# Kernel optimization log

Measured on AMD Instinct MI355X. Metric: run time of the kernel, lower is better.

The kernel has to match this reference:

```python
import jax, jax.numpy as jnp
import numpy as np

B, C, H, W = 4, 256, 64, 64
C8 = C // 8


def _xavier(key, shape):
    fan_in, fan_out = shape[1], shape[0]
    limit = float(np.sqrt(6.0 / (fan_in + fan_out)))
    return jax.random.uniform(key, shape, jnp.float32, -limit, limit)


def setup_inputs() -> dict:
    key = jax.random.key(0)
    ks = jax.random.split(key, 10)
    inp = {
        "x": jax.random.normal(ks[0], (B, C, H, W), jnp.float32),
        "y": jax.random.normal(ks[1], (B, C, H, W), jnp.float32),
        "Wfx": _xavier(ks[2], (C8, C)), "bfx": jnp.zeros((C8,), jnp.float32),
        "Wgx": _xavier(ks[3], (C8, C)), "bgx": jnp.zeros((C8,), jnp.float32),
        "Whx": _xavier(ks[4], (C, C)),  "bhx": jnp.zeros((C,), jnp.float32),
        "Wfy": _xavier(ks[5], (C8, C)), "bfy": jnp.zeros((C8,), jnp.float32),
        "Wgy": _xavier(ks[6], (C8, C)), "bgy": jnp.zeros((C8,), jnp.float32),
        "Why": _xavier(ks[7], (C, C)),  "bhy": jnp.zeros((C,), jnp.float32),
        # torch init is gamma=0 which zeroes the attention branch; use a random
        # scalar so the reference exercises the full computation.
        "gamma": jax.random.normal(ks[8], (1,), jnp.float32),
    }
    return inp


def _conv1x1(x, Wt, b):
    # 1x1 conv == per-pixel linear over channels; output flattened to [B, O, N]
    b_, c, h, w = x.shape
    out = jnp.einsum('oc,bchw->bohw', Wt, x) + b[None, :, None, None]
    return out.reshape(b_, -1, h * w)


def reference(x, y, Wfx, bfx, Wgx, bgx, Whx, bhx, Wfy, bfy, Wgy, bgy, Why, bhy, gamma):
    b, c, h, w = x.shape
    fx = _conv1x1(x, Wfx, bfx)  # [B, C8, N]
    gx = _conv1x1(x, Wgx, bgx)
    hx = _conv1x1(x, Whx, bhx)  # [B, C, N]
    fy = _conv1x1(y, Wfy, bfy)
    gy = _conv1x1(y, Wgy, bgy)
    hy = _conv1x1(y, Why, bhy)

    # attention_x = softmax(f_y^T @ g_x) over last dim; [B, N, N]
    att_x = jax.nn.softmax(jnp.einsum('bcn,bcm->bnm', fy, gx), axis=-1)
    att_y = jax.nn.softmax(jnp.einsum('bcn,bcm->bnm', fx, gy), axis=-1)

    sa_x = jnp.einsum('bcn,bnm->bcm', hx, att_x).reshape(b, c, h, w)
    sa_y = jnp.einsum('bcn,bnm->bcm', hy, att_y).reshape(b, c, h, w)

    out_x = gamma[0] * sa_x + x
    out_y = gamma[0] * sa_y + y
    return (out_x, out_y)
```

## Files before the change

kernel.cpp:

```cpp
#include <hip/hip_runtime.h>

#define BB 4
#define CC 256
#define NN 4096

typedef _Float16 half_t;
typedef __attribute__((ext_vector_type(8))) _Float16 half8;
typedef __attribute__((ext_vector_type(4))) _Float16 half4;
typedef __attribute__((ext_vector_type(4))) float floatx4;
typedef __attribute__((ext_vector_type(16))) float floatx16;

__global__ __launch_bounds__(256)
void cvt_w_kernel(const float* __restrict__ Wfx, const float* __restrict__ Wgx,
                  const float* __restrict__ Whx, const float* __restrict__ Wfy,
                  const float* __restrict__ Wgy, const float* __restrict__ Why,
                  half_t* __restrict__ oWfx, half_t* __restrict__ oWgx,
                  half_t* __restrict__ oWhx, half_t* __restrict__ oWfy,
                  half_t* __restrict__ oWgy, half_t* __restrict__ oWhy)
{
    const float* src; half_t* dst; int n;
    switch (blockIdx.y) {
        case 0: src = Wfx; dst = oWfx; n = 32 * CC; break;
        case 1: src = Wgx; dst = oWgx; n = 32 * CC; break;
        case 2: src = Whx; dst = oWhx; n = CC * CC; break;
        case 3: src = Wfy; dst = oWfy; n = 32 * CC; break;
        case 4: src = Wgy; dst = oWgy; n = 32 * CC; break;
        default: src = Why; dst = oWhy; n = CC * CC; break;
    }
    int idx = (blockIdx.x * 256 + threadIdx.x) * 4;
    if (idx >= n) return;
    float4 v = *(const float4*)&src[idx];
    half4 h; h[0] = (half_t)v.x; h[1] = (half_t)v.y; h[2] = (half_t)v.z; h[3] = (half_t)v.w;
    *(half4*)&dst[idx] = h;
}

__global__ __launch_bounds__(512, 4)
void prep_kernel(const float* __restrict__ x, const float* __restrict__ y,
                 const half_t* __restrict__ Wfx, const half_t* __restrict__ Wgx,
                 const half_t* __restrict__ Whx, const half_t* __restrict__ Wfy,
                 const half_t* __restrict__ Wgy, const half_t* __restrict__ Why,
                 const float* __restrict__ bfx, const float* __restrict__ bgx,
                 const float* __restrict__ bhx, const float* __restrict__ bfy,
                 const float* __restrict__ bgy, const float* __restrict__ bhy,
                 half_t* __restrict__ fxT, half_t* __restrict__ gxT,
                 half_t* __restrict__ hx,
                 half_t* __restrict__ fyT, half_t* __restrict__ gyT,
                 half_t* __restrict__ hy)
{
    __shared__ half_t xT[64][266];

    const int n0 = blockIdx.x * 64;
    const int b  = blockIdx.y;
    const int sel = blockIdx.z;
    const float* in = sel ? y : x;
    const half_t* Wf = sel ? Wfy : Wfx;
    const half_t* Wg = sel ? Wgy : Wgx;
    const half_t* Wh = sel ? Why : Whx;
    const float*  bf = sel ? bfy : bfx;
    const float*  bg = sel ? bgy : bgx;
    const float*  bh = sel ? bhy : bhx;
    half_t* fT = sel ? fyT : fxT;
    half_t* gT = sel ? gyT : gxT;
    half_t* h  = sel ? hy : hx;

    const int t = threadIdx.x;
    const int w = t >> 6, lane = t & 63;
    const int q = lane >> 4, mc = lane & 15;

    {
        const int n4 = t & 15;
        const int cb = t >> 4;
        const float* inb = in + (size_t)b * CC * NN + n0 + n4 * 4;
        #pragma unroll
        for (int j = 0; j < 8; ++j) {
            const int c = cb + 32 * j;
            float4 v = *(const float4*)&inb[(size_t)c * NN];
            xT[n4 * 4 + 0][c] = (half_t)v.x;
            xT[n4 * 4 + 1][c] = (half_t)v.y;
            xT[n4 * 4 + 2][c] = (half_t)v.z;
            xT[n4 * 4 + 3][c] = (half_t)v.w;
        }
    }
    __syncthreads();

    {
        const int of  = w >> 1;
        const int col = (of & 1) * 16 + mc;
        const half_t* Ws = (of < 2) ? Wf : Wg;
        const float*  bs = (of < 2) ? bf : bg;
        half_t* dst = (of < 2) ? fT : gT;
        const float bv = bs[col];
        floatx4 accf[2] = {{bv, bv, bv, bv}, {bv, bv, bv, bv}};

        #pragma unroll
        for (int ks = 0; ks < 8; ++ks) {
            int k0 = ks * 32 + q * 8;
            half8 bfr = *(const half8*)&Ws[(size_t)col * CC + k0];
            #pragma unroll
            for (int e = 0; e < 2; ++e) {
                half8 af = *(const half8*)&xT[(w & 1) * 32 + e * 16 + mc][k0];
                accf[e] = __builtin_amdgcn_mfma_f32_16x16x32_f16(af, bfr, accf[e], 0, 0, 0);
            }
        }
        #pragma unroll
        for (int e = 0; e < 2; ++e)
            #pragma unroll
            for (int r = 0; r < 4; ++r) {
                int n = n0 + (w & 1) * 32 + e * 16 + q * 4 + r;
                dst[((size_t)b * NN + n) * 32 + col] = (half_t)accf[e][r];
            }
    }

    {
        const int o0 = w * 32;
        floatx4 acch[2][4];
        #pragma unroll
        for (int j = 0; j < 2; ++j) {
            floatx4 bv;
            #pragma unroll
            for (int r = 0; r < 4; ++r) bv[r] = bh[o0 + j * 16 + q * 4 + r];
            #pragma unroll
            for (int i = 0; i < 4; ++i) acch[j][i] = bv;
        }

        #pragma unroll
        for (int ks = 0; ks < 8; ++ks) {
            int k0 = ks * 32 + q * 8;
            half8 a0 = *(const half8*)&Wh[(size_t)(o0 + mc) * CC + k0];
            half8 a1 = *(const half8*)&Wh[(size_t)(o0 + 16 + mc) * CC + k0];
            #pragma unroll
            for (int i = 0; i < 4; ++i) {
                half8 bfr = *(const half8*)&xT[i * 16 + mc][k0];
                acch[0][i] = __builtin_amdgcn_mfma_f32_16x16x32_f16(a0, bfr, acch[0][i], 0, 0, 0);
                acch[1][i] = __builtin_amdgcn_mfma_f32_16x16x32_f16(a1, bfr, acch[1][i], 0, 0, 0);
            }
        }

        half_t* hb = h + (size_t)b * CC * NN;
        #pragma unroll
        for (int j = 0; j < 2; ++j)
            #pragma unroll
            for (int i = 0; i < 4; ++i)
                #pragma unroll
                for (int r = 0; r < 4; ++r) {
                    int o = o0 + j * 16 + q * 4 + r;
                    hb[(size_t)o * NN + n0 + i * 16 + mc] = (half_t)acch[j][i][r];
                }
    }
}

__global__ __launch_bounds__(256)
void stats_kernel(const half_t* __restrict__ fT0, const half_t* __restrict__ gT0,
                  const half_t* __restrict__ fT1, const half_t* __restrict__ gT1,
                  float* __restrict__ L0, float* __restrict__ L1)
{
    __shared__ float red_l[4][32];
    const int b  = blockIdx.y;
    const int sel = blockIdx.z;
    const half_t* fT = sel ? fT1 : fT0;
    const half_t* gT = sel ? gT1 : gT0;
    float* Lout = sel ? L1 : L0;

    const int n0 = blockIdx.x * 32;
    const int t  = threadIdx.x;
    const int w = t >> 6, lane = t & 63, q = lane >> 4, mc = lane & 15;
    const half_t* fTb = fT + (size_t)b * NN * 32;
    const half_t* gTb = gT + (size_t)b * NN * 32;

    half8 a0 = *(const half8*)&fTb[(size_t)(n0 + mc) * 32 + q * 8];
    half8 a1 = *(const half8*)&fTb[(size_t)(n0 + 16 + mc) * 32 + q * 8];

    float l0[4] = {0.f, 0.f, 0.f, 0.f}, l1[4] = {0.f, 0.f, 0.f, 0.f};
    for (int it = 0; it < NN / 64; ++it) {
        int m = (it * 4 + w) * 16 + mc;
        half8 bfr = *(const half8*)&gTb[(size_t)m * 32 + q * 8];
        floatx4 S0 = __builtin_amdgcn_mfma_f32_16x16x32_f16(a0, bfr, (floatx4){0.f,0.f,0.f,0.f}, 0, 0, 0);
        floatx4 S1 = __builtin_amdgcn_mfma_f32_16x16x32_f16(a1, bfr, (floatx4){0.f,0.f,0.f,0.f}, 0, 0, 0);
        #pragma unroll
        for (int r = 0; r < 4; ++r) { l0[r] += __expf(S0[r]); l1[r] += __expf(S1[r]); }
    }
    #pragma unroll
    for (int r = 0; r < 4; ++r) {
        #pragma unroll
        for (int off = 1; off < 16; off <<= 1) {
            l0[r] += __shfl_xor(l0[r], off);
            l1[r] += __shfl_xor(l1[r], off);
        }
    }
    if (mc == 0)
        #pragma unroll
        for (int r = 0; r < 4; ++r) {
            red_l[w][q * 4 + r]      = l0[r];
            red_l[w][16 + q * 4 + r] = l1[r];
        }
    __syncthreads();
    if (t < 32) {
        float L = red_l[0][t] + red_l[1][t] + red_l[2][t] + red_l[3][t];
        Lout[(size_t)b * NN + n0 + t] = -log2f(L);
    }
}

__global__ __launch_bounds__(512, 4)
void pv_kernel(const half_t* __restrict__ fT0, const half_t* __restrict__ gT0,
               const half_t* __restrict__ h0, const float* __restrict__ L0,
               const float* __restrict__ src0, float* __restrict__ out0,
               const half_t* __restrict__ fT1, const half_t* __restrict__ gT1,
               const half_t* __restrict__ h1, const float* __restrict__ L1,
               const float* __restrict__ src1, float* __restrict__ out1,
               const float* __restrict__ gamma)
{
    __shared__ half_t h_lds[256][72];
    __shared__ half_t PT[2][64][72];

    const int m0 = blockIdx.x * 64;
    const int b  = blockIdx.y & 3;
    const int sel = blockIdx.y >> 2;
    const half_t* fT = sel ? fT1 : fT0;
    const half_t* gT = sel ? gT1 : gT0;
    const half_t* h  = sel ? h1 : h0;
    const float*  Lg = sel ? L1 : L0;
    const float*  src = sel ? src1 : src0;
    float* out = sel ? out1 : out0;

    const int t = threadIdx.x;
    const int w = t >> 6, lane = t & 63;
    const int q = lane >> 4, mc = lane & 15;
    const int l5 = lane >> 5, l31 = lane & 31;

    const int mg  = (w >> 1) * 16;
    const int nhf = (w & 1) * 32;

    const half_t* fTb = fT + (size_t)b * NN * 32;
    const half_t* gTb = gT + (size_t)b * NN * 32;
    const half_t* hb  = h + (size_t)b * CC * NN;
    const float*  Lb  = Lg + (size_t)b * NN;

    const half8 gS = *(const half8*)&gTb[(size_t)(m0 + mg + mc) * 32 + q * 8];

    const int srow = t >> 3;
    const int sch  = t & 7;

    const half_t* hP = hb + (size_t)srow * NN + sch * 8;
    const half_t* fP = fTb + (size_t)(nhf + mc) * 32 + q * 8;
    const float*  lP = Lb + nhf + q * 4;

    floatx16 acc[2];
    #pragma unroll
    for (int bm = 0; bm < 2; ++bm)
        #pragma unroll
        for (int r = 0; r < 16; ++r) acc[bm][r] = 0.f;

    half8 hpre[4];
    half8 fu[2], ff[2];
    floatx4 lvu[2], lvf[2];

    {
        half8 f0[2]; floatx4 l0[2];
        #pragma unroll
        for (int s = 0; s < 2; ++s) {
            f0[s] = *(const half8*)&fP[(size_t)(s * 16) * 32];
            l0[s] = *(const floatx4*)&lP[s * 16];
        }
        #pragma unroll
        for (int s = 0; s < 2; ++s) {
            floatx4 S = __builtin_amdgcn_mfma_f32_16x16x32_f16(
                f0[s], gS, (floatx4){0.f, 0.f, 0.f, 0.f}, 0, 0, 0);
            half4 p;
            p[0] = (half_t)exp2f(fmaf(S[0], 1.44269504f, l0[s][0]));
            p[1] = (half_t)exp2f(fmaf(S[1], 1.44269504f, l0[s][1]));
            p[2] = (half_t)exp2f(fmaf(S[2], 1.44269504f, l0[s][2]));
            p[3] = (half_t)exp2f(fmaf(S[3], 1.44269504f, l0[s][3]));
            *(half4*)&PT[0][mg + mc][nhf + s * 16 + q * 4] = p;
        }
    }
    #pragma unroll
    for (int i = 0; i < 4; ++i)
        hpre[i] = *(const half8*)&hP[(size_t)(64 * i) * NN];
    #pragma unroll
    for (int s = 0; s < 2; ++s) {
        fu[s]  = *(const half8*)&fP[(size_t)(64 + s * 16) * 32];
        lvu[s] = *(const floatx4*)&lP[64 + s * 16];
    }

    #pragma unroll 2
    for (int T = 0; T < NN / 64; ++T) {
        const int cur = T & 1, nxt = cur ^ 1;

        __syncthreads();
        #pragma unroll
        for (int i = 0; i < 4; ++i)
            *(half8*)&h_lds[srow + 64 * i][sch * 8] = hpre[i];
        __syncthreads();

        int ntn  = (T + 1) * 64; if (ntn  >= NN) ntn  = 0;
        int ntn2 = (T + 2) * 64; if (ntn2 >= NN) ntn2 -= NN;
        #pragma unroll
        for (int i = 0; i < 4; ++i)
            hpre[i] = *(const half8*)&hP[(size_t)(64 * i) * NN + ntn];
        #pragma unroll
        for (int s = 0; s < 2; ++s) {
            ff[s]  = *(const half8*)&fP[(size_t)(ntn2 + s * 16) * 32];
            lvf[s] = *(const floatx4*)&lP[ntn2 + s * 16];
        }

        #pragma unroll
        for (int s = 0; s < 2; ++s) {
            floatx4 S = __builtin_amdgcn_mfma_f32_16x16x32_f16(
                fu[s], gS, (floatx4){0.f, 0.f, 0.f, 0.f}, 0, 0, 0);
            half4 p;
            p[0] = (half_t)exp2f(fmaf(S[0], 1.44269504f, lvu[s][0]));
            p[1] = (half_t)exp2f(fmaf(S[1], 1.44269504f, lvu[s][1]));
            p[2] = (half_t)exp2f(fmaf(S[2], 1.44269504f, lvu[s][2]));
            p[3] = (half_t)exp2f(fmaf(S[3], 1.44269504f, lvu[s][3]));
            *(half4*)&PT[nxt][mg + mc][nhf + s * 16 + q * 4] = p;
        }

        __builtin_amdgcn_s_setprio(1);
        #pragma unroll
        for (int ch = 0; ch < 4; ++ch) {
            half8 Ah = *(const half8*)&h_lds[w * 32 + l31][ch * 16 + l5 * 8];
            half8 B0 = *(const half8*)&PT[cur][l31][ch * 16 + l5 * 8];
            half8 B1 = *(const half8*)&PT[cur][32 + l31][ch * 16 + l5 * 8];
            acc[0] = __builtin_amdgcn_mfma_f32_32x32x16_f16(Ah, B0, acc[0], 0, 0, 0);
            acc[1] = __builtin_amdgcn_mfma_f32_32x32x16_f16(Ah, B1, acc[1], 0, 0, 0);
        }
        __builtin_amdgcn_s_setprio(0);

        #pragma unroll
        for (int s = 0; s < 2; ++s) { fu[s] = ff[s]; lvu[s] = lvf[s]; }
    }

    const float gm = gamma[0];
    const float* srcb = src + (size_t)b * CC * NN;
    float* outb = out + (size_t)b * CC * NN;
    #pragma unroll
    for (int bm = 0; bm < 2; ++bm) {
        const int m = m0 + bm * 32 + l31;
        #pragma unroll
        for (int r = 0; r < 16; ++r) {
            int c = w * 32 + (r & 3) + 8 * (r >> 2) + 4 * l5;
            size_t idx = (size_t)c * NN + m;
            outb[idx] = fmaf(gm, acc[bm][r], srcb[idx]);
        }
    }
}

extern "C" void kernel_launch(void* const* d_in, const int* in_sizes, int n_in,
                              void* d_out, int out_size, void* d_ws, size_t ws_size,
                              hipStream_t stream)
{
    const float* x   = (const float*)d_in[0];
    const float* y   = (const float*)d_in[1];
    const float* Wfx = (const float*)d_in[2];
    const float* bfx = (const float*)d_in[3];
    const float* Wgx = (const float*)d_in[4];
    const float* bgx = (const float*)d_in[5];
    const float* Whx = (const float*)d_in[6];
    const float* bhx = (const float*)d_in[7];
    const float* Wfy = (const float*)d_in[8];
    const float* bfy = (const float*)d_in[9];
    const float* Wgy = (const float*)d_in[10];
    const float* bgy = (const float*)d_in[11];
    const float* Why = (const float*)d_in[12];
    const float* bhy = (const float*)d_in[13];
    const float* gam = (const float*)d_in[14];

    const size_t SZ_XT = (size_t)BB * NN * CC;
    const size_t SZ_FG = (size_t)BB * NN * 32;
    half_t* xTx   = (half_t*)d_ws;
    half_t* xTy   = xTx + SZ_XT;
    half_t* hx    = xTy + SZ_XT;
    half_t* hy    = hx + SZ_XT;
    half_t* fxT   = hy + SZ_XT;
    half_t* gxT   = fxT + SZ_FG;
    half_t* fyT   = gxT + SZ_FG;
    half_t* gyT   = fyT + SZ_FG;
    half_t* Wfx_h = gyT + SZ_FG;
    half_t* Wgx_h = Wfx_h + 32 * CC;
    half_t* Wfy_h = Wgx_h + 32 * CC;
    half_t* Wgy_h = Wfy_h + 32 * CC;
    half_t* Whx_h = Wgy_h + 32 * CC;
    half_t* Why_h = Whx_h + CC * CC;
    float*  Lx    = (float*)(Why_h + CC * CC);
    float*  Ly    = Lx + (size_t)BB * NN;

    float* outx = (float*)d_out;
    float* outy = outx + (size_t)BB * CC * NN;

    cvt_w_kernel<<<dim3(64, 6), 256, 0, stream>>>(Wfx, Wgx, Whx, Wfy, Wgy, Why,
                                                  Wfx_h, Wgx_h, Whx_h, Wfy_h, Wgy_h, Why_h);

    prep_kernel<<<dim3(64, 4, 2), 512, 0, stream>>>(
        x, y, Wfx_h, Wgx_h, Whx_h, Wfy_h, Wgy_h, Why_h,
        bfx, bgx, bhx, bfy, bgy, bhy,
        fxT, gxT, hx, fyT, gyT, hy);

    stats_kernel<<<dim3(128, 4, 2), 256, 0, stream>>>(fyT, gxT, fxT, gyT, Lx, Ly);

    pv_kernel<<<dim3(64, 8), 512, 0, stream>>>(
        fyT, gxT, hx, Lx, x, outx,
        fxT, gyT, hy, Ly, y, outy, gam);
}
```

Before: 253.4 us.

## Double the PV kernel output tile to 128 columns to reuse staged h tiles

The PV kernel now covers 128 output positions per block instead of 64. Each wave computes a 2x2 grid of 32x32 MFMA tiles, and the QK/exp stage produces two 16-row slices per wave. This halves how often the h tile is reloaded from global memory per output and raises MFMA work per LDS load. In exchange the grid shrinks to 256 blocks, the launch bound drops to 2 blocks per CU, and more accumulator registers and LDS are used per block, so latency hiding may get worse.

```diff
diff --git a/kernel.cpp b/kernel.cpp
--- a/kernel.cpp
+++ b/kernel.cpp
@@ -200,7 +200,7 @@
     }
 }
 
-__global__ __launch_bounds__(512, 4)
+__global__ __launch_bounds__(512, 2)
 void pv_kernel(const half_t* __restrict__ fT0, const half_t* __restrict__ gT0,
                const half_t* __restrict__ h0, const float* __restrict__ L0,
                const float* __restrict__ src0, float* __restrict__ out0,
@@ -210,9 +210,9 @@
                const float* __restrict__ gamma)
 {
     __shared__ half_t h_lds[256][72];
-    __shared__ half_t PT[2][64][72];
-
-    const int m0 = blockIdx.x * 64;
+    __shared__ half_t PT[2][128][72];
+
+    const int m0 = blockIdx.x * 128;
     const int b  = blockIdx.y & 3;
     const int sel = blockIdx.y >> 2;
     const half_t* fT = sel ? fT1 : fT0;
@@ -227,28 +227,34 @@
     const int q = lane >> 4, mc = lane & 15;
     const int l5 = lane >> 5, l31 = lane & 31;
 
-    const int mg  = (w >> 1) * 16;
-    const int nhf = (w & 1) * 32;
+    const int smg = (w >> 1) * 32;
+    const int snh = (w & 1) * 32;
+    const int cg  = (w & 3) * 64;
+    const int pmg = (w >> 2) * 64;
 
     const half_t* fTb = fT + (size_t)b * NN * 32;
     const half_t* gTb = gT + (size_t)b * NN * 32;
     const half_t* hb  = h + (size_t)b * CC * NN;
     const float*  Lb  = Lg + (size_t)b * NN;
 
-    const half8 gS = *(const half8*)&gTb[(size_t)(m0 + mg + mc) * 32 + q * 8];
+    half8 gS[2];
+    gS[0] = *(const half8*)&gTb[(size_t)(m0 + smg + mc) * 32 + q * 8];
+    gS[1] = *(const half8*)&gTb[(size_t)(m0 + smg + 16 + mc) * 32 + q * 8];
 
     const int srow = t >> 3;
     const int sch  = t & 7;
 
     const half_t* hP = hb + (size_t)srow * NN + sch * 8;
-    const half_t* fP = fTb + (size_t)(nhf + mc) * 32 + q * 8;
-    const float*  lP = Lb + nhf + q * 4;
-
-    floatx16 acc[2];
+    const half_t* fP = fTb + (size_t)(snh + mc) * 32 + q * 8;
+    const float*  lP = Lb + snh + q * 4;
+
+    floatx16 acc[2][2];
     #pragma unroll
-    for (int bm = 0; bm < 2; ++bm)
-        #pragma unroll
-        for (int r = 0; r < 16; ++r) acc[bm][r] = 0.f;
+    for (int a = 0; a < 2; ++a)
+        #pragma unroll
+        for (int ms = 0; ms < 2; ++ms)
+            #pragma unroll
+            for (int r = 0; r < 16; ++r) acc[a][ms][r] = 0.f;
 
     half8 hpre[4];
     half8 fu[2], ff[2];
@@ -262,16 +268,18 @@
             l0[s] = *(const floatx4*)&lP[s * 16];
         }
         #pragma unroll
-        for (int s = 0; s < 2; ++s) {
-            floatx4 S = __builtin_amdgcn_mfma_f32_16x16x32_f16(
-                f0[s], gS, (floatx4){0.f, 0.f, 0.f, 0.f}, 0, 0, 0);
-            half4 p;
-            p[0] = (half_t)exp2f(fmaf(S[0], 1.44269504f, l0[s][0]));
-            p[1] = (half_t)exp2f(fmaf(S[1], 1.44269504f, l0[s][1]));
-            p[2] = (half_t)exp2f(fmaf(S[2], 1.44269504f, l0[s][2]));
-            p[3] = (half_t)exp2f(fmaf(S[3], 1.44269504f, l0[s][3]));
-            *(half4*)&PT[0][mg + mc][nhf + s * 16 + q * 4] = p;
-        }
+        for (int u = 0; u < 2; ++u)
+            #pragma unroll
+            for (int s = 0; s < 2; ++s) {
+                floatx4 S = __builtin_amdgcn_mfma_f32_16x16x32_f16(
+                    f0[s], gS[u], (floatx4){0.f, 0.f, 0.f, 0.f}, 0, 0, 0);
+                half4 p;
+                p[0] = (half_t)exp2f(fmaf(S[0], 1.44269504f, l0[s][0]));
+                p[1] = (half_t)exp2f(fmaf(S[1], 1.44269504f, l0[s][1]));
+                p[2] = (half_t)exp2f(fmaf(S[2], 1.44269504f, l0[s][2]));
+                p[3] = (half_t)exp2f(fmaf(S[3], 1.44269504f, l0[s][3]));
+                *(half4*)&PT[0][smg + u * 16 + mc][snh + s * 16 + q * 4] = p;
+            }
     }
     #pragma unroll
     for (int i = 0; i < 4; ++i)
@@ -304,25 +312,30 @@
         }
 
         #pragma unroll
-        for (int s = 0; s < 2; ++s) {
-            floatx4 S = __builtin_amdgcn_mfma_f32_16x16x32_f16(
-                fu[s], gS, (floatx4){0.f, 0.f, 0.f, 0.f}, 0, 0, 0);
-            half4 p;
-            p[0] = (half_t)exp2f(fmaf(S[0], 1.44269504f, lvu[s][0]));
-            p[1] = (half_t)exp2f(fmaf(S[1], 1.44269504f, lvu[s][1]));
-            p[2] = (half_t)exp2f(fmaf(S[2], 1.44269504f, lvu[s][2]));
-            p[3] = (half_t)exp2f(fmaf(S[3], 1.44269504f, lvu[s][3]));
-            *(half4*)&PT[nxt][mg + mc][nhf + s * 16 + q * 4] = p;
-        }
+        for (int u = 0; u < 2; ++u)
+            #pragma unroll
+            for (int s = 0; s < 2; ++s) {
+                floatx4 S = __builtin_amdgcn_mfma_f32_16x16x32_f16(
+                    fu[s], gS[u], (floatx4){0.f, 0.f, 0.f, 0.f}, 0, 0, 0);
+                half4 p;
+                p[0] = (half_t)exp2f(fmaf(S[0], 1.44269504f, lvu[s][0]));
+                p[1] = (half_t)exp2f(fmaf(S[1], 1.44269504f, lvu[s][1]));
+                p[2] = (half_t)exp2f(fmaf(S[2], 1.44269504f, lvu[s][2]));
+                p[3] = (half_t)exp2f(fmaf(S[3], 1.44269504f, lvu[s][3]));
+                *(half4*)&PT[nxt][smg + u * 16 + mc][snh + s * 16 + q * 4] = p;
+            }
 
         __builtin_amdgcn_s_setprio(1);
         #pragma unroll
         for (int ch = 0; ch < 4; ++ch) {
-            half8 Ah = *(const half8*)&h_lds[w * 32 + l31][ch * 16 + l5 * 8];
-            half8 B0 = *(const half8*)&PT[cur][l31][ch * 16 + l5 * 8];
-            half8 B1 = *(const half8*)&PT[cur][32 + l31][ch * 16 + l5 * 8];
-            acc[0] = __builtin_amdgcn_mfma_f32_32x32x16_f16(Ah, B0, acc[0], 0, 0, 0);
-            acc[1] = __builtin_amdgcn_mfma_f32_32x32x16_f16(Ah, B1, acc[1], 0, 0, 0);
+            half8 A0 = *(const half8*)&h_lds[cg + l31][ch * 16 + l5 * 8];
+            half8 A1 = *(const half8*)&h_lds[cg + 32 + l31][ch * 16 + l5 * 8];
+            half8 B0 = *(const half8*)&PT[cur][pmg + l31][ch * 16 + l5 * 8];
+            half8 B1 = *(const half8*)&PT[cur][pmg + 32 + l31][ch * 16 + l5 * 8];
+            acc[0][0] = __builtin_amdgcn_mfma_f32_32x32x16_f16(A0, B0, acc[0][0], 0, 0, 0);
+            acc[0][1] = __builtin_amdgcn_mfma_f32_32x32x16_f16(A0, B1, acc[0][1], 0, 0, 0);
+            acc[1][0] = __builtin_amdgcn_mfma_f32_32x32x16_f16(A1, B0, acc[1][0], 0, 0, 0);
+            acc[1][1] = __builtin_amdgcn_mfma_f32_32x32x16_f16(A1, B1, acc[1][1], 0, 0, 0);
         }
         __builtin_amdgcn_s_setprio(0);
 
@@ -334,15 +347,17 @@
     const float* srcb = src + (size_t)b * CC * NN;
     float* outb = out + (size_t)b * CC * NN;
     #pragma unroll
-    for (int bm = 0; bm < 2; ++bm) {
-        const int m = m0 + bm * 32 + l31;
-        #pragma unroll
-        for (int r = 0; r < 16; ++r) {
-            int c = w * 32 + (r & 3) + 8 * (r >> 2) + 4 * l5;
-            size_t idx = (size_t)c * NN + m;
-            outb[idx] = fmaf(gm, acc[bm][r], srcb[idx]);
-        }
-    }
+    for (int a = 0; a < 2; ++a)
+        #pragma unroll
+        for (int ms = 0; ms < 2; ++ms) {
+            const int m = m0 + pmg + ms * 32 + l31;
+            #pragma unroll
+            for (int r = 0; r < 16; ++r) {
+                int c = cg + a * 32 + (r & 3) + 8 * (r >> 2) + 4 * l5;
+                size_t idx = (size_t)c * NN + m;
+                outb[idx] = fmaf(gm, acc[a][ms][r], srcb[idx]);
+            }
+        }
 }
 
 extern "C" void kernel_launch(void* const* d_in, const int* in_sizes, int n_in,
@@ -397,7 +412,7 @@
 
     stats_kernel<<<dim3(128, 4, 2), 256, 0, stream>>>(fyT, gxT, fxT, gyT, Lx, Ly);
 
-    pv_kernel<<<dim3(64, 8), 512, 0, stream>>>(
+    pv_kernel<<<dim3(32, 8), 512, 0, stream>>>(
         fyT, gxT, hx, Lx, x, outx,
         fxT, gyT, hy, Ly, y, outy, gam);
 }
```

Measured after the change: 249.2 us. About the same (-1.7%).

## Store h in MFMA-fragment layout and load PV A-operands directly from global

Applied to the files above, without the earlier changes.

The projection kernel now writes h in a tiled layout of 16-element chunks grouped by 64-pixel tile and channel, so the PV kernel can load its MFMA A fragments straight from global memory into registers instead of staging h through a 36KB LDS buffer. The PV loop is restructured: each warp now covers 64 channels by 32 pixels (two accumulators sharing one P fragment), the h LDS store and one of the two barriers per iteration are removed, and the loop is manually unrolled by two via a macro. This cuts LDS traffic and footprint, which may raise occupancy, but the global A loads are issued in the same iteration they are consumed, which exposes their latency with no prefetch distance.

```diff
diff --git a/kernel.cpp b/kernel.cpp
--- a/kernel.cpp
+++ b/kernel.cpp
@@ -113,6 +113,7 @@
 
     {
         const int o0 = w * 32;
+        const int Tt = n0 >> 6;
         floatx4 acch[2][4];
         #pragma unroll
         for (int j = 0; j < 2; ++j) {
@@ -136,7 +137,7 @@
             }
         }
 
-        half_t* hb = h + (size_t)b * CC * NN;
+        half_t* hb = h + (size_t)b * NN * CC;
         #pragma unroll
         for (int j = 0; j < 2; ++j)
             #pragma unroll
@@ -144,7 +145,7 @@
                 #pragma unroll
                 for (int r = 0; r < 4; ++r) {
                     int o = o0 + j * 16 + q * 4 + r;
-                    hb[(size_t)o * NN + n0 + i * 16 + mc] = (half_t)acch[j][i][r];
+                    hb[((size_t)((Tt * 4 + i) * 256 + o) << 4) + mc] = (half_t)acch[j][i][r];
                 }
     }
 }
@@ -202,14 +203,13 @@
 
 __global__ __launch_bounds__(512, 4)
 void pv_kernel(const half_t* __restrict__ fT0, const half_t* __restrict__ gT0,
-               const half_t* __restrict__ h0, const float* __restrict__ L0,
+               const half_t* __restrict__ hF0, const float* __restrict__ L0,
                const float* __restrict__ src0, float* __restrict__ out0,
                const half_t* __restrict__ fT1, const half_t* __restrict__ gT1,
-               const half_t* __restrict__ h1, const float* __restrict__ L1,
+               const half_t* __restrict__ hF1, const float* __restrict__ L1,
                const float* __restrict__ src1, float* __restrict__ out1,
                const float* __restrict__ gamma)
 {
-    __shared__ half_t h_lds[256][72];
     __shared__ half_t PT[2][64][72];
 
     const int m0 = blockIdx.x * 64;
@@ -217,7 +217,7 @@
     const int sel = blockIdx.y >> 2;
     const half_t* fT = sel ? fT1 : fT0;
     const half_t* gT = sel ? gT1 : gT0;
-    const half_t* h  = sel ? h1 : h0;
+    const half_t* hF = sel ? hF1 : hF0;
     const float*  Lg = sel ? L1 : L0;
     const float*  src = sel ? src1 : src0;
     float* out = sel ? out1 : out0;
@@ -227,32 +227,31 @@
     const int q = lane >> 4, mc = lane & 15;
     const int l5 = lane >> 5, l31 = lane & 31;
 
-    const int mg  = (w >> 1) * 16;
-    const int nhf = (w & 1) * 32;
+    const int smg = (w >> 1) * 16;
+    const int snh = (w & 1) * 32;
+    const int cg  = (w & 3) * 64;
+    const int mg  = (w >> 2) * 32;
 
     const half_t* fTb = fT + (size_t)b * NN * 32;
     const half_t* gTb = gT + (size_t)b * NN * 32;
-    const half_t* hb  = h + (size_t)b * CC * NN;
+    const half_t* hFb = hF + (size_t)b * NN * CC;
     const float*  Lb  = Lg + (size_t)b * NN;
 
-    const half8 gS = *(const half8*)&gTb[(size_t)(m0 + mg + mc) * 32 + q * 8];
-
-    const int srow = t >> 3;
-    const int sch  = t & 7;
-
-    const half_t* hP = hb + (size_t)srow * NN + sch * 8;
-    const half_t* fP = fTb + (size_t)(nhf + mc) * 32 + q * 8;
-    const float*  lP = Lb + nhf + q * 4;
+    const half8 gS = *(const half8*)&gTb[(size_t)(m0 + smg + mc) * 32 + q * 8];
+
+    const half_t* aP = hFb + (size_t)(cg + l31) * 16 + l5 * 8;
+    const half_t* fP = fTb + (size_t)(snh + mc) * 32 + q * 8;
+    const float*  lP = Lb + snh + q * 4;
 
     floatx16 acc[2];
     #pragma unroll
-    for (int bm = 0; bm < 2; ++bm)
-        #pragma unroll
-        for (int r = 0; r < 16; ++r) acc[bm][r] = 0.f;
-
-    half8 hpre[4];
-    half8 fu[2], ff[2];
-    floatx4 lvu[2], lvf[2];
+    for (int a = 0; a < 2; ++a)
+        #pragma unroll
+        for (int r = 0; r < 16; ++r) acc[a][r] = 0.f;
+
+    half8 Ar[2][4];
+    half8 fr[2][2];
+    floatx4 lr[2][2];
 
     {
         half8 f0[2]; floatx4 l0[2];
@@ -270,79 +269,69 @@
             p[1] = (half_t)exp2f(fmaf(S[1], 1.44269504f, l0[s][1]));
             p[2] = (half_t)exp2f(fmaf(S[2], 1.44269504f, l0[s][2]));
             p[3] = (half_t)exp2f(fmaf(S[3], 1.44269504f, l0[s][3]));
-            *(half4*)&PT[0][mg + mc][nhf + s * 16 + q * 4] = p;
-        }
-    }
-    #pragma unroll
-    for (int i = 0; i < 4; ++i)
-        hpre[i] = *(const half8*)&hP[(size_t)(64 * i) * NN];
+            *(half4*)&PT[0][smg + mc][snh + s * 16 + q * 4] = p;
+        }
+    }
     #pragma unroll
     for (int s = 0; s < 2; ++s) {
-        fu[s]  = *(const half8*)&fP[(size_t)(64 + s * 16) * 32];
-        lvu[s] = *(const floatx4*)&lP[64 + s * 16];
-    }
-
-    #pragma unroll 2
-    for (int T = 0; T < NN / 64; ++T) {
-        const int cur = T & 1, nxt = cur ^ 1;
-
-        __syncthreads();
-        #pragma unroll
-        for (int i = 0; i < 4; ++i)
-            *(half8*)&h_lds[srow + 64 * i][sch * 8] = hpre[i];
-        __syncthreads();
-
-        int ntn  = (T + 1) * 64; if (ntn  >= NN) ntn  = 0;
-        int ntn2 = (T + 2) * 64; if (ntn2 >= NN) ntn2 -= NN;
-        #pragma unroll
-        for (int i = 0; i < 4; ++i)
-            hpre[i] = *(const half8*)&hP[(size_t)(64 * i) * NN + ntn];
-        #pragma unroll
-        for (int s = 0; s < 2; ++s) {
-            ff[s]  = *(const half8*)&fP[(size_t)(ntn2 + s * 16) * 32];
-            lvf[s] = *(const floatx4*)&lP[ntn2 + s * 16];
-        }
-
-        #pragma unroll
-        for (int s = 0; s < 2; ++s) {
-            floatx4 S = __builtin_amdgcn_mfma_f32_16x16x32_f16(
-                fu[s], gS, (floatx4){0.f, 0.f, 0.f, 0.f}, 0, 0, 0);
-            half4 p;
-            p[0] = (half_t)exp2f(fmaf(S[0], 1.44269504f, lvu[s][0]));
-            p[1] = (half_t)exp2f(fmaf(S[1], 1.44269504f, lvu[s][1]));
-            p[2] = (half_t)exp2f(fmaf(S[2], 1.44269504f, lvu[s][2]));
-            p[3] = (half_t)exp2f(fmaf(S[3], 1.44269504f, lvu[s][3]));
-            *(half4*)&PT[nxt][mg + mc][nhf + s * 16 + q * 4] = p;
-        }
-
-        __builtin_amdgcn_s_setprio(1);
-        #pragma unroll
-        for (int ch = 0; ch < 4; ++ch) {
-            half8 Ah = *(const half8*)&h_lds[w * 32 + l31][ch * 16 + l5 * 8];
-            half8 B0 = *(const half8*)&PT[cur][l31][ch * 16 + l5 * 8];
-            half8 B1 = *(const half8*)&PT[cur][32 + l31][ch * 16 + l5 * 8];
-            acc[0] = __builtin_amdgcn_mfma_f32_32x32x16_f16(Ah, B0, acc[0], 0, 0, 0);
-            acc[1] = __builtin_amdgcn_mfma_f32_32x32x16_f16(Ah, B1, acc[1], 0, 0, 0);
-        }
-        __builtin_amdgcn_s_setprio(0);
-
-        #pragma unroll
-        for (int s = 0; s < 2; ++s) { fu[s] = ff[s]; lvu[s] = lvf[s]; }
-    }
+        fr[0][s] = *(const half8*)&fP[(size_t)(64 + s * 16) * 32];
+        lr[0][s] = *(const floatx4*)&lP[64 + s * 16];
+    }
+    __syncthreads();
+
+#define PVBODY(T, par, opp) {                                                 \
+    const int T2_ = ((T) + 2) & 63;                                           \
+    _Pragma("unroll")                                                         \
+    for (int a_ = 0; a_ < 2; ++a_)                                            \
+        _Pragma("unroll")                                                     \
+        for (int c_ = 0; c_ < 4; ++c_)                                        \
+            Ar[a_][c_] = *(const half8*)&aP[((size_t)((T) * 4 + c_) << 12) + a_ * 512]; \
+    _Pragma("unroll")                                                         \
+    for (int s_ = 0; s_ < 2; ++s_) {                                          \
+        fr[opp][s_] = *(const half8*)&fP[(size_t)(T2_ * 64 + s_ * 16) * 32];  \
+        lr[opp][s_] = *(const floatx4*)&lP[T2_ * 64 + s_ * 16];               \
+    }                                                                         \
+    _Pragma("unroll")                                                         \
+    for (int s_ = 0; s_ < 2; ++s_) {                                          \
+        floatx4 S_ = __builtin_amdgcn_mfma_f32_16x16x32_f16(                  \
+            fr[par][s_], gS, (floatx4){0.f, 0.f, 0.f, 0.f}, 0, 0, 0);         \
+        half4 p_;                                                             \
+        p_[0] = (half_t)exp2f(fmaf(S_[0], 1.44269504f, lr[par][s_][0]));      \
+        p_[1] = (half_t)exp2f(fmaf(S_[1], 1.44269504f, lr[par][s_][1]));      \
+        p_[2] = (half_t)exp2f(fmaf(S_[2], 1.44269504f, lr[par][s_][2]));      \
+        p_[3] = (half_t)exp2f(fmaf(S_[3], 1.44269504f, lr[par][s_][3]));      \
+        *(half4*)&PT[opp][smg + mc][snh + s_ * 16 + q * 4] = p_;              \
+    }                                                                         \
+    __builtin_amdgcn_s_setprio(1);                                            \
+    _Pragma("unroll")                                                         \
+    for (int c_ = 0; c_ < 4; ++c_) {                                          \
+        half8 B_ = *(const half8*)&PT[par][mg + l31][c_ * 16 + l5 * 8];       \
+        acc[0] = __builtin_amdgcn_mfma_f32_32x32x16_f16(Ar[0][c_], B_, acc[0], 0, 0, 0); \
+        acc[1] = __builtin_amdgcn_mfma_f32_32x32x16_f16(Ar[1][c_], B_, acc[1], 0, 0, 0); \
+    }                                                                         \
+    __builtin_amdgcn_s_setprio(0);                                            \
+    __syncthreads();                                                          \
+}
+
+    for (int T = 0; T < NN / 64; T += 2) {
+        PVBODY(T, 0, 1);
+        PVBODY(T + 1, 1, 0);
+    }
+
+#undef PVBODY
 
     const float gm = gamma[0];
     const float* srcb = src + (size_t)b * CC * NN;
     float* outb = out + (size_t)b * CC * NN;
+    const int m = m0 + mg + l31;
     #pragma unroll
-    for (int bm = 0; bm < 2; ++bm) {
-        const int m = m0 + bm * 32 + l31;
+    for (int a = 0; a < 2; ++a)
         #pragma unroll
         for (int r = 0; r < 16; ++r) {
-            int c = w * 32 + (r & 3) + 8 * (r >> 2) + 4 * l5;
+            int c = cg + a * 32 + (r & 3) + 8 * (r >> 2) + 4 * l5;
             size_t idx = (size_t)c * NN + m;
-            outb[idx] = fmaf(gm, acc[bm][r], srcb[idx]);
-        }
-    }
+            outb[idx] = fmaf(gm, acc[a][r], srcb[idx]);
+        }
 }
 
 extern "C" void kernel_launch(void* const* d_in, const int* in_sizes, int n_in,
```

Result: slower. 273.3 us (+7.9%).
